# Performance work log

Measured on AMD Instinct MI355X. Metric: run time of the kernel, lower is better.

## Reference

```python
import jax, jax.numpy as jnp
import numpy as np
from jax import lax

DB4 = np.array([0.2303778133088964, 0.7148465705529155, 0.6308807679298587,
                -0.027983769416859854, -0.18703481171888114, 0.030841381835986965,
                0.032883011666982945, -0.010597401785069032], dtype=np.float32)


def _make_filters():
    h = DB4
    g = np.array([(-1) ** n * DB4[7 - n] for n in range(8)], dtype=np.float32)
    # analysis filters (as in DaubechiesDWT): [LL, LH, HL, HH], each 8x8
    anal = np.stack([np.outer(h, h), np.outer(h, g), np.outer(g, h), np.outer(g, g)], axis=0)
    anal = anal[:, None, :, :]  # (4,1,8,8) OIHW depthwise
    # synthesis filters (as in DaubechiesIDWT), built from time-reversed filters
    h_r, g_r = h[::-1], g[::-1]
    syn = np.stack([np.outer(h_r, h_r), np.outer(h_r, g_r), np.outer(g_r, h_r), np.outer(g_r, g_r)], axis=0)
    syn = syn[:, None, :, :]  # (4,1,8,8), torch conv_transpose weight layout (IC, OC/g, kH, kW)
    # convert conv_transpose2d(stride=2, pad=3) to a dilated conv: flip spatially, swap I/O,
    # equivalent padding = k - 1 - pad = 8 - 1 - 3 = 4
    syn_eq = np.transpose(syn[:, :, ::-1, ::-1], (1, 0, 2, 3)).copy()  # (1,4,8,8) OIHW
    return jnp.asarray(anal), jnp.asarray(syn_eq)


def setup_inputs() -> dict:
    key = jax.random.key(0)
    x = jax.random.normal(key, (32, 3, 512, 512), dtype=jnp.float32)
    return {"x": x}


def reference(x) -> jnp.ndarray:
    B, C, H, W = x.shape
    anal_w, syn_w = _make_filters()
    dn = ('NCHW', 'OIHW', 'NCHW')
    # --- depthwise DWT: groups=C, stride 2, pad 3 -> (B, 4C, Ho, Wo) ---
    anal_wC = jnp.tile(anal_w, (C, 1, 1, 1))  # (4C,1,8,8)
    coeffs = lax.conv_general_dilated(x, anal_wC, window_strides=(2, 2),
                                      padding=[(3, 3), (3, 3)],
                                      feature_group_count=C, dimension_numbers=dn)
    Ho, Wo = coeffs.shape[-2], coeffs.shape[-1]
    coeffs = coeffs.reshape(B, C, 4, Ho, Wo)
    # --- high-pass: zero the LL subband ---
    coeffs = coeffs.at[:, :, 0].set(0.0)
    coeffs = coeffs.reshape(B, 4 * C, Ho, Wo)
    # --- IDWT as single grouped transposed conv (lhs_dilation=2, pad 4) ---
    syn_wC = jnp.tile(syn_w, (C, 1, 1, 1))  # (C,4,8,8)
    recon = lax.conv_general_dilated(coeffs, syn_wC, window_strides=(1, 1),
                                     padding=[(4, 4), (4, 4)], lhs_dilation=(2, 2),
                                     feature_group_count=C, dimension_numbers=dn)
    recon = recon[:, :, :2 * Ho, :2 * Wo]  # crop to output_size = (2*Ho, 2*Wo)
    # --- per-sample min-max normalization ---
    mn = jnp.min(recon, axis=(1, 2, 3), keepdims=True)
    mx = jnp.max(recon, axis=(1, 2, 3), keepdims=True)
    return (recon - mn) / (mx - mn + 1e-8)
```

## Files before the change

kernel.cpp:

```cpp
#include <hip/hip_runtime.h>

#define H0 0.2303778133088964f
#define H1 0.7148465705529155f
#define H2 0.6308807679298587f
#define H3 (-0.027983769416859854f)
#define H4 (-0.18703481171888114f)
#define H5 0.030841381835986965f
#define H6 0.032883011666982945f
#define H7 (-0.010597401785069032f)


__global__ __launch_bounds__(256, 8) void dwt_fused_k(const float* __restrict__ x,
                                                      float* __restrict__ out,
                                                      float* __restrict__ pmn,
                                                      float* __restrict__ pmx) {
    constexpr float h[8] = {H0, H1, H2, H3, H4, H5, H6, H7};
    constexpr float g[8] = {H7, -H6, H5, -H4, H3, -H2, H1, -H0};

    const int tileX = blockIdx.x;
    const int tileY = blockIdx.y;
    const int img = blockIdx.z;
    const int N0 = tileX * 32;
    const int M0 = tileY * 32;
    const int tid = threadIdx.x;

    __shared__ __align__(16) unsigned char smem[16928];
    float* sx = (float*)smem;
    float* y1 = (float*)smem;
    float* y2 = (float*)(smem + 1600);
    float* y3 = (float*)(smem + 3200);
    float* red = (float*)(smem + 4800);
    float* uL = (float*)(smem + 9568);
    float* uH = (float*)(smem + 13248);
    float* sP = (float*)(smem + 9568);
    float* sQ = (float*)(smem + 12128);

    const float* xp = x + (size_t)img * (512 * 512);

    {
        const int gr0 = M0 - 7, gc0 = N0 - 8;
        for (int k = tid; k < 598; k += 256) {
            int row = k / 13;
            int c4 = k - row * 13;
            int gr = gr0 + row;
            int gc = gc0 + 4 * c4;
            float4 v = make_float4(0.f, 0.f, 0.f, 0.f);
            if ((unsigned)gr < 512u && (unsigned)gc < 512u)
                v = *(const float4*)(xp + gr * 512 + gc);
            *(float4*)(sx + row * 52 + 4 * c4) = v;
        }
    }
    __syncthreads();

    const int C0 = (N0 >> 1) - 2;
    if (tid < 230) {
        int p = tid / 5;
        int q = tid - p * 5;
        const float4* wr = (const float4*)(sx + p * 52 + 8 * q);
        float4 w0 = wr[0], w1 = wr[1], w2 = wr[2], w3 = wr[3];
        float W[16] = {w0.x, w0.y, w0.z, w0.w, w1.x, w1.y, w1.z, w1.w,
                       w2.x, w2.y, w2.z, w2.w, w3.x, w3.y, w3.z, w3.w};
        float aL[4] = {0.f, 0.f, 0.f, 0.f}, aH[4] = {0.f, 0.f, 0.f, 0.f};
#pragma unroll
        for (int d = 0; d < 4; ++d) {
#pragma unroll
            for (int j = 0; j < 8; ++j) {
                float v = W[1 + 2 * d + j];
                aL[d] += h[j] * v;
                aH[d] += g[j] * v;
            }
            if ((unsigned)(C0 + 4 * q + d) >= 256u) { aL[d] = 0.f; aH[d] = 0.f; }
        }
        *(float4*)(uL + p * 20 + 4 * q) = make_float4(aL[0], aL[1], aL[2], aL[3]);
        *(float4*)(uH + p * 20 + 4 * q) = make_float4(aH[0], aH[1], aH[2], aH[3]);
    }
    __syncthreads();

    const int R0 = (M0 >> 1) - 2;
    if (tid < 100) {
        int lr = tid / 5;
        int q = tid - lr * 5;
        float a1[4] = {0.f, 0.f, 0.f, 0.f};
        float a2[4] = {0.f, 0.f, 0.f, 0.f};
        float a3[4] = {0.f, 0.f, 0.f, 0.f};
        if ((unsigned)(R0 + lr) < 256u) {
#pragma unroll
            for (int i = 0; i < 8; ++i) {
                float4 vH = *(const float4*)(uH + (2 * lr + i) * 20 + 4 * q);
                float4 vL = *(const float4*)(uL + (2 * lr + i) * 20 + 4 * q);
                a1[0] += h[i] * vH.x; a1[1] += h[i] * vH.y; a1[2] += h[i] * vH.z; a1[3] += h[i] * vH.w;
                a2[0] += g[i] * vL.x; a2[1] += g[i] * vL.y; a2[2] += g[i] * vL.z; a2[3] += g[i] * vL.w;
                a3[0] += g[i] * vH.x; a3[1] += g[i] * vH.y; a3[2] += g[i] * vH.z; a3[3] += g[i] * vH.w;
            }
        }
        *(float4*)(y1 + lr * 20 + 4 * q) = make_float4(a1[0], a1[1], a1[2], a1[3]);
        *(float4*)(y2 + lr * 20 + 4 * q) = make_float4(a2[0], a2[1], a2[2], a2[3]);
        *(float4*)(y3 + lr * 20 + 4 * q) = make_float4(a3[0], a3[1], a3[2], a3[3]);
    }
    __syncthreads();

    if (tid < 160) {
        int m = tid / 5;
        int q = tid - m * 5;
        int mh = (m + (m & 1)) >> 1;
        int t0 = m & 1;
        float ch0 = t0 ? H1 : H0, ch1 = t0 ? H3 : H2, ch2 = t0 ? H5 : H4, ch3 = t0 ? H7 : H6;
        float cg0 = t0 ? -H6 : H7, cg1 = t0 ? -H4 : H5, cg2 = t0 ? -H2 : H3, cg3 = t0 ? -H0 : H1;
        float P[4] = {0.f, 0.f, 0.f, 0.f}, Q[4] = {0.f, 0.f, 0.f, 0.f};
#pragma unroll
        for (int k = 0; k < 4; ++k) {
            float chk = (k == 0) ? ch0 : (k == 1) ? ch1 : (k == 2) ? ch2 : ch3;
            float cgk = (k == 0) ? cg0 : (k == 1) ? cg1 : (k == 2) ? cg2 : cg3;
            float4 v1 = *(const float4*)(y1 + (mh + k) * 20 + 4 * q);
            float4 v3 = *(const float4*)(y3 + (mh + k) * 20 + 4 * q);
            float4 v2 = *(const float4*)(y2 + (mh + k) * 20 + 4 * q);
            P[0] += chk * v1.x + cgk * v3.x; P[1] += chk * v1.y + cgk * v3.y;
            P[2] += chk * v1.z + cgk * v3.z; P[3] += chk * v1.w + cgk * v3.w;
            Q[0] += cgk * v2.x; Q[1] += cgk * v2.y; Q[2] += cgk * v2.z; Q[3] += cgk * v2.w;
        }
        *(float4*)(sP + m * 20 + 4 * q) = make_float4(P[0], P[1], P[2], P[3]);
        *(float4*)(sQ + m * 20 + 4 * q) = make_float4(Q[0], Q[1], Q[2], Q[3]);
    }
    __syncthreads();

    float lmn = 3.4e38f, lmx = -3.4e38f;
    if (tid < 128) {
        int m = tid >> 2;
        int qq = tid & 3;
        const float* pp = sP + m * 20 + 4 * qq;
        const float* qp = sQ + m * 20 + 4 * qq;
        float4 pa = *(const float4*)pp, pb = *(const float4*)(pp + 4);
        float4 qa = *(const float4*)qp, qb = *(const float4*)(qp + 4);
        float sp[8] = {pa.x, pa.y, pa.z, pa.w, pb.x, pb.y, pb.z, pb.w};
        float sq[8] = {qa.x, qa.y, qa.z, qa.w, qb.x, qb.y, qb.z, qb.w};
        float val[8];
#pragma unroll
        for (int e = 0; e < 8; ++e) {
            const int t0 = e & 1;
            const int r0 = (e + (e & 1)) >> 1;
            float r = g[t0] * sp[r0] + g[t0 + 2] * sp[r0 + 1] + g[t0 + 4] * sp[r0 + 2] + g[t0 + 6] * sp[r0 + 3]
                    + h[t0] * sq[r0] + h[t0 + 2] * sq[r0 + 1] + h[t0 + 4] * sq[r0 + 2] + h[t0 + 6] * sq[r0 + 3];
            val[e] = r;
            lmn = fminf(lmn, r);
            lmx = fmaxf(lmx, r);
        }
        float* op = out + ((size_t)img * 512 + (M0 + m)) * 512 + (N0 + 8 * qq);
        *(float4*)op = make_float4(val[0], val[1], val[2], val[3]);
        *(float4*)(op + 4) = make_float4(val[4], val[5], val[6], val[7]);
    }

#pragma unroll
    for (int off = 32; off > 0; off >>= 1) {
        lmn = fminf(lmn, __shfl_down(lmn, off));
        lmx = fmaxf(lmx, __shfl_down(lmx, off));
    }
    int wv = tid >> 6;
    if ((tid & 63) == 0) { red[wv] = lmn; red[4 + wv] = lmx; }
    __syncthreads();
    if (tid == 0) {
        float mn = fminf(fminf(red[0], red[1]), fminf(red[2], red[3]));
        float mx = fmaxf(fmaxf(red[4], red[5]), fmaxf(red[6], red[7]));
        int blin = (img * 16 + tileY) * 16 + tileX;
        pmn[blin] = mn;
        pmx[blin] = mx;
    }
}

__global__ __launch_bounds__(256) void minmax_reduce_k(const float* __restrict__ pmn,
                                                       const float* __restrict__ pmx,
                                                       float* __restrict__ mnmx) {
    __shared__ float r[8];
    int s = blockIdx.x;
    int tid = threadIdx.x;
    int base = s * 768;
    float lmn = 3.4e38f, lmx = -3.4e38f;
#pragma unroll
    for (int k = 0; k < 3; ++k) {
        lmn = fminf(lmn, pmn[base + tid + 256 * k]);
        lmx = fmaxf(lmx, pmx[base + tid + 256 * k]);
    }
#pragma unroll
    for (int off = 32; off > 0; off >>= 1) {
        lmn = fminf(lmn, __shfl_down(lmn, off));
        lmx = fmaxf(lmx, __shfl_down(lmx, off));
    }
    int wv = tid >> 6;
    if ((tid & 63) == 0) { r[wv] = lmn; r[4 + wv] = lmx; }
    __syncthreads();
    if (tid == 0) {
        mnmx[s]      = fminf(fminf(r[0], r[1]), fminf(r[2], r[3]));
        mnmx[32 + s] = fmaxf(fmaxf(r[4], r[5]), fmaxf(r[6], r[7]));
    }
}

__global__ __launch_bounds__(256) void normalize_k(float* __restrict__ out,
                                                   const float* __restrict__ mnmx) {
    int t = blockIdx.x * 256 + threadIdx.x;
    float4* o4 = (float4*)out;
#pragma unroll
    for (int it = 0; it < 6; ++it) {
        size_t i = (size_t)t + (size_t)it * 1048576;
        int s = (int)(i / 196608);
        float mn = mnmx[s];
        float mx = mnmx[32 + s];
        float inv = 1.0f / (mx - mn + 1e-8f);
        float4 v = o4[i];
        v.x = (v.x - mn) * inv;
        v.y = (v.y - mn) * inv;
        v.z = (v.z - mn) * inv;
        v.w = (v.w - mn) * inv;
        o4[i] = v;
    }
}

extern "C" void kernel_launch(void* const* d_in, const int* in_sizes, int n_in,
                              void* d_out, int out_size, void* d_ws, size_t ws_size,
                              hipStream_t stream) {
    const float* x = (const float*)d_in[0];
    float* out = (float*)d_out;
    float* wsf = (float*)d_ws;
    float* pmn = wsf;
    float* pmx = wsf + 24576;
    float* mnmx = wsf + 49152;

    hipLaunchKernelGGL(dwt_fused_k, dim3(16, 16, 96), dim3(256), 0, stream, x, out, pmn, pmx);
    hipLaunchKernelGGL(minmax_reduce_k, dim3(32), dim3(256), 0, stream, pmn, pmx, mnmx);
    hipLaunchKernelGGL(normalize_k, dim3(4096), dim3(256), 0, stream, out, mnmx);
}
```

Measured before the change: 241.1 us.

## Widen DWT tiles to 64 columns and fold min-max reduction into normalize

```diff
diff --git a/kernel.cpp b/kernel.cpp
--- a/kernel.cpp
+++ b/kernel.cpp
@@ -9,8 +9,7 @@
 #define H6 0.032883011666982945f
 #define H7 (-0.010597401785069032f)
 
-
-__global__ __launch_bounds__(256, 8) void dwt_fused_k(const float* __restrict__ x,
+__global__ __launch_bounds__(256, 5) void dwt_fused_k(const float* __restrict__ x,
                                                       float* __restrict__ out,
                                                       float* __restrict__ pmn,
                                                       float* __restrict__ pmx) {
@@ -20,43 +19,43 @@
     const int tileX = blockIdx.x;
     const int tileY = blockIdx.y;
     const int img = blockIdx.z;
-    const int N0 = tileX * 32;
+    const int N0 = tileX * 64;
     const int M0 = tileY * 32;
     const int tid = threadIdx.x;
 
-    __shared__ __align__(16) unsigned char smem[16928];
+    __shared__ __align__(16) unsigned char smem[27968];
     float* sx = (float*)smem;
     float* y1 = (float*)smem;
-    float* y2 = (float*)(smem + 1600);
-    float* y3 = (float*)(smem + 3200);
-    float* red = (float*)(smem + 4800);
-    float* uL = (float*)(smem + 9568);
-    float* uH = (float*)(smem + 13248);
-    float* sP = (float*)(smem + 9568);
-    float* sQ = (float*)(smem + 12128);
+    float* y2 = (float*)(smem + 2880);
+    float* y3 = (float*)(smem + 5760);
+    float* red = (float*)(smem + 8640);
+    float* uL = (float*)(smem + 14720);
+    float* uH = (float*)(smem + 21344);
+    float* sP = (float*)(smem + 14720);
+    float* sQ = (float*)(smem + 19328);
 
     const float* xp = x + (size_t)img * (512 * 512);
 
     {
         const int gr0 = M0 - 7, gc0 = N0 - 8;
-        for (int k = tid; k < 598; k += 256) {
-            int row = k / 13;
-            int c4 = k - row * 13;
+        for (int k = tid; k < 920; k += 256) {
+            int row = k / 20;
+            int c4 = k - row * 20;
             int gr = gr0 + row;
             int gc = gc0 + 4 * c4;
             float4 v = make_float4(0.f, 0.f, 0.f, 0.f);
             if ((unsigned)gr < 512u && (unsigned)gc < 512u)
                 v = *(const float4*)(xp + gr * 512 + gc);
-            *(float4*)(sx + row * 52 + 4 * c4) = v;
+            *(float4*)(sx + row * 80 + 4 * c4) = v;
         }
     }
     __syncthreads();
 
     const int C0 = (N0 >> 1) - 2;
-    if (tid < 230) {
-        int p = tid / 5;
-        int q = tid - p * 5;
-        const float4* wr = (const float4*)(sx + p * 52 + 8 * q);
+    for (int t = tid; t < 414; t += 256) {
+        int p = t / 9;
+        int gq = t - p * 9;
+        const float4* wr = (const float4*)(sx + p * 80 + 8 * gq);
         float4 w0 = wr[0], w1 = wr[1], w2 = wr[2], w3 = wr[3];
         float W[16] = {w0.x, w0.y, w0.z, w0.w, w1.x, w1.y, w1.z, w1.w,
                        w2.x, w2.y, w2.z, w2.w, w3.x, w3.y, w3.z, w3.w};
@@ -69,39 +68,39 @@
                 aL[d] += h[j] * v;
                 aH[d] += g[j] * v;
             }
-            if ((unsigned)(C0 + 4 * q + d) >= 256u) { aL[d] = 0.f; aH[d] = 0.f; }
-        }
-        *(float4*)(uL + p * 20 + 4 * q) = make_float4(aL[0], aL[1], aL[2], aL[3]);
-        *(float4*)(uH + p * 20 + 4 * q) = make_float4(aH[0], aH[1], aH[2], aH[3]);
+            if ((unsigned)(C0 + 4 * gq + d) >= 256u) { aL[d] = 0.f; aH[d] = 0.f; }
+        }
+        *(float4*)(uL + p * 36 + 4 * gq) = make_float4(aL[0], aL[1], aL[2], aL[3]);
+        *(float4*)(uH + p * 36 + 4 * gq) = make_float4(aH[0], aH[1], aH[2], aH[3]);
     }
     __syncthreads();
 
     const int R0 = (M0 >> 1) - 2;
-    if (tid < 100) {
-        int lr = tid / 5;
-        int q = tid - lr * 5;
+    if (tid < 180) {
+        int lr = tid / 9;
+        int gq = tid - lr * 9;
         float a1[4] = {0.f, 0.f, 0.f, 0.f};
         float a2[4] = {0.f, 0.f, 0.f, 0.f};
         float a3[4] = {0.f, 0.f, 0.f, 0.f};
         if ((unsigned)(R0 + lr) < 256u) {
 #pragma unroll
             for (int i = 0; i < 8; ++i) {
-                float4 vH = *(const float4*)(uH + (2 * lr + i) * 20 + 4 * q);
-                float4 vL = *(const float4*)(uL + (2 * lr + i) * 20 + 4 * q);
+                float4 vH = *(const float4*)(uH + (2 * lr + i) * 36 + 4 * gq);
+                float4 vL = *(const float4*)(uL + (2 * lr + i) * 36 + 4 * gq);
                 a1[0] += h[i] * vH.x; a1[1] += h[i] * vH.y; a1[2] += h[i] * vH.z; a1[3] += h[i] * vH.w;
                 a2[0] += g[i] * vL.x; a2[1] += g[i] * vL.y; a2[2] += g[i] * vL.z; a2[3] += g[i] * vL.w;
                 a3[0] += g[i] * vH.x; a3[1] += g[i] * vH.y; a3[2] += g[i] * vH.z; a3[3] += g[i] * vH.w;
             }
         }
-        *(float4*)(y1 + lr * 20 + 4 * q) = make_float4(a1[0], a1[1], a1[2], a1[3]);
-        *(float4*)(y2 + lr * 20 + 4 * q) = make_float4(a2[0], a2[1], a2[2], a2[3]);
-        *(float4*)(y3 + lr * 20 + 4 * q) = make_float4(a3[0], a3[1], a3[2], a3[3]);
-    }
-    __syncthreads();
-
-    if (tid < 160) {
-        int m = tid / 5;
-        int q = tid - m * 5;
+        *(float4*)(y1 + lr * 36 + 4 * gq) = make_float4(a1[0], a1[1], a1[2], a1[3]);
+        *(float4*)(y2 + lr * 36 + 4 * gq) = make_float4(a2[0], a2[1], a2[2], a2[3]);
+        *(float4*)(y3 + lr * 36 + 4 * gq) = make_float4(a3[0], a3[1], a3[2], a3[3]);
+    }
+    __syncthreads();
+
+    for (int t = tid; t < 288; t += 256) {
+        int m = t / 9;
+        int gq = t - m * 9;
         int mh = (m + (m & 1)) >> 1;
         int t0 = m & 1;
         float ch0 = t0 ? H1 : H0, ch1 = t0 ? H3 : H2, ch2 = t0 ? H5 : H4, ch3 = t0 ? H7 : H6;
@@ -111,24 +110,24 @@
         for (int k = 0; k < 4; ++k) {
             float chk = (k == 0) ? ch0 : (k == 1) ? ch1 : (k == 2) ? ch2 : ch3;
             float cgk = (k == 0) ? cg0 : (k == 1) ? cg1 : (k == 2) ? cg2 : cg3;
-            float4 v1 = *(const float4*)(y1 + (mh + k) * 20 + 4 * q);
-            float4 v3 = *(const float4*)(y3 + (mh + k) * 20 + 4 * q);
-            float4 v2 = *(const float4*)(y2 + (mh + k) * 20 + 4 * q);
+            float4 v1 = *(const float4*)(y1 + (mh + k) * 36 + 4 * gq);
+            float4 v3 = *(const float4*)(y3 + (mh + k) * 36 + 4 * gq);
+            float4 v2 = *(const float4*)(y2 + (mh + k) * 36 + 4 * gq);
             P[0] += chk * v1.x + cgk * v3.x; P[1] += chk * v1.y + cgk * v3.y;
             P[2] += chk * v1.z + cgk * v3.z; P[3] += chk * v1.w + cgk * v3.w;
             Q[0] += cgk * v2.x; Q[1] += cgk * v2.y; Q[2] += cgk * v2.z; Q[3] += cgk * v2.w;
         }
-        *(float4*)(sP + m * 20 + 4 * q) = make_float4(P[0], P[1], P[2], P[3]);
-        *(float4*)(sQ + m * 20 + 4 * q) = make_float4(Q[0], Q[1], Q[2], Q[3]);
+        *(float4*)(sP + m * 36 + 4 * gq) = make_float4(P[0], P[1], P[2], P[3]);
+        *(float4*)(sQ + m * 36 + 4 * gq) = make_float4(Q[0], Q[1], Q[2], Q[3]);
     }
     __syncthreads();
 
     float lmn = 3.4e38f, lmx = -3.4e38f;
-    if (tid < 128) {
-        int m = tid >> 2;
-        int qq = tid & 3;
-        const float* pp = sP + m * 20 + 4 * qq;
-        const float* qp = sQ + m * 20 + 4 * qq;
+    {
+        int m = tid >> 3;
+        int qq = tid & 7;
+        const float* pp = sP + m * 36 + 4 * qq;
+        const float* qp = sQ + m * 36 + 4 * qq;
         float4 pa = *(const float4*)pp, pb = *(const float4*)(pp + 4);
         float4 qa = *(const float4*)qp, qb = *(const float4*)(qp + 4);
         float sp[8] = {pa.x, pa.y, pa.z, pa.w, pb.x, pb.y, pb.z, pb.w};
@@ -160,24 +159,27 @@
     if (tid == 0) {
         float mn = fminf(fminf(red[0], red[1]), fminf(red[2], red[3]));
         float mx = fmaxf(fmaxf(red[4], red[5]), fmaxf(red[6], red[7]));
-        int blin = (img * 16 + tileY) * 16 + tileX;
+        int blin = (img * 16 + tileY) * 8 + tileX;
         pmn[blin] = mn;
         pmx[blin] = mx;
     }
 }
 
-__global__ __launch_bounds__(256) void minmax_reduce_k(const float* __restrict__ pmn,
-                                                       const float* __restrict__ pmx,
-                                                       float* __restrict__ mnmx) {
+__global__ __launch_bounds__(256) void normalize_k(float* __restrict__ out,
+                                                   const float* __restrict__ pmn,
+                                                   const float* __restrict__ pmx) {
     __shared__ float r[8];
-    int s = blockIdx.x;
-    int tid = threadIdx.x;
-    int base = s * 768;
+    __shared__ float bc[2];
+    const int b = blockIdx.x;
+    const int s = b / 96;
+    const int chunk = b - s * 96;
+    const int tid = threadIdx.x;
+
     float lmn = 3.4e38f, lmx = -3.4e38f;
-#pragma unroll
-    for (int k = 0; k < 3; ++k) {
-        lmn = fminf(lmn, pmn[base + tid + 256 * k]);
-        lmx = fmaxf(lmx, pmx[base + tid + 256 * k]);
+    const int base = s * 384;
+    for (int j = tid; j < 384; j += 256) {
+        lmn = fminf(lmn, pmn[base + j]);
+        lmx = fmaxf(lmx, pmx[base + j]);
     }
 #pragma unroll
     for (int off = 32; off > 0; off >>= 1) {
@@ -188,22 +190,18 @@
     if ((tid & 63) == 0) { r[wv] = lmn; r[4 + wv] = lmx; }
     __syncthreads();
     if (tid == 0) {
-        mnmx[s]      = fminf(fminf(r[0], r[1]), fminf(r[2], r[3]));
-        mnmx[32 + s] = fmaxf(fmaxf(r[4], r[5]), fmaxf(r[6], r[7]));
-    }
-}
-
-__global__ __launch_bounds__(256) void normalize_k(float* __restrict__ out,
-                                                   const float* __restrict__ mnmx) {
-    int t = blockIdx.x * 256 + threadIdx.x;
+        bc[0] = fminf(fminf(r[0], r[1]), fminf(r[2], r[3]));
+        bc[1] = fmaxf(fmaxf(r[4], r[5]), fmaxf(r[6], r[7]));
+    }
+    __syncthreads();
+    const float mn = bc[0];
+    const float inv = 1.0f / (bc[1] - mn + 1e-8f);
+
     float4* o4 = (float4*)out;
-#pragma unroll
-    for (int it = 0; it < 6; ++it) {
-        size_t i = (size_t)t + (size_t)it * 1048576;
-        int s = (int)(i / 196608);
-        float mn = mnmx[s];
-        float mx = mnmx[32 + s];
-        float inv = 1.0f / (mx - mn + 1e-8f);
+    const size_t base4 = (size_t)s * 196608 + (size_t)chunk * 2048;
+#pragma unroll
+    for (int it = 0; it < 8; ++it) {
+        size_t i = base4 + it * 256 + tid;
         float4 v = o4[i];
         v.x = (v.x - mn) * inv;
         v.y = (v.y - mn) * inv;
@@ -220,10 +218,8 @@
     float* out = (float*)d_out;
     float* wsf = (float*)d_ws;
     float* pmn = wsf;
-    float* pmx = wsf + 24576;
-    float* mnmx = wsf + 49152;
-
-    hipLaunchKernelGGL(dwt_fused_k, dim3(16, 16, 96), dim3(256), 0, stream, x, out, pmn, pmx);
-    hipLaunchKernelGGL(minmax_reduce_k, dim3(32), dim3(256), 0, stream, pmn, pmx, mnmx);
-    hipLaunchKernelGGL(normalize_k, dim3(4096), dim3(256), 0, stream, out, mnmx);
+    float* pmx = wsf + 12288;
+
+    hipLaunchKernelGGL(dwt_fused_k, dim3(8, 16, 96), dim3(256), 0, stream, x, out, pmn, pmx);
+    hipLaunchKernelGGL(normalize_k, dim3(3072), dim3(256), 0, stream, out, pmn, pmx);
 }
```

New measurement: 250.2 us. +3.8%, slower.

## Fold vertical IDWT/DWT passes into precomputed combined taps for interior tiles

Applied to the files above, without the earlier changes.

```diff
diff --git a/kernel.cpp b/kernel.cpp
--- a/kernel.cpp
+++ b/kernel.cpp
@@ -9,8 +9,33 @@
 #define H6 0.032883011666982945f
 #define H7 (-0.010597401785069032f)
 
-
-__global__ __launch_bounds__(256, 8) void dwt_fused_k(const float* __restrict__ x,
+struct Taps { float cp[2][14]; float cq[2][14]; };
+constexpr Taps mk_taps() {
+    Taps t{};
+    const float h[8] = {H0, H1, H2, H3, H4, H5, H6, H7};
+    const float g[8] = {H7, -H6, H5, -H4, H3, -H2, H1, -H0};
+    for (int par = 0; par < 2; ++par)
+        for (int j = 0; j < 14; ++j) {
+            float cp = 0.f, cq = 0.f;
+            for (int k = 0; k < 4; ++k) {
+                int i = j - 2 * k;
+                if (i >= 0 && i < 8) {
+                    cp += h[2 * k + par] * h[i] + g[2 * k + par] * g[i];
+                    cq += g[2 * k + par] * g[i];
+                }
+            }
+            t.cp[par][j] = cp;
+            t.cq[par][j] = cq;
+        }
+    return t;
+}
+constexpr Taps TAPS = mk_taps();
+
+__device__ __forceinline__ int uoff(int r, int c4) {
+    return r * 32 + 4 * (c4 ^ ((r >> 1) & 7));
+}
+
+__global__ __launch_bounds__(256, 7) void dwt_fused_k(const float* __restrict__ x,
                                                       float* __restrict__ out,
                                                       float* __restrict__ pmn,
                                                       float* __restrict__ pmx) {
@@ -24,16 +49,22 @@
     const int M0 = tileY * 32;
     const int tid = threadIdx.x;
 
-    __shared__ __align__(16) unsigned char smem[16928];
+    __shared__ __align__(16) unsigned char smem[21344];
     float* sx = (float*)smem;
     float* y1 = (float*)smem;
     float* y2 = (float*)(smem + 1600);
     float* y3 = (float*)(smem + 3200);
-    float* red = (float*)(smem + 4800);
+    float* red = (float*)(smem + 5120);
     float* uL = (float*)(smem + 9568);
-    float* uH = (float*)(smem + 13248);
-    float* sP = (float*)(smem + 9568);
-    float* sQ = (float*)(smem + 12128);
+    float* uH = (float*)(smem + 15456);
+    float* sPi = (float*)smem;
+    float* sQi = (float*)(smem + 2560);
+    float* sPb = (float*)(smem + 9568);
+    float* sQb = (float*)(smem + 12128);
+
+    const bool boundary = (tileY == 0) | (tileY == 15);
+    float* sP = boundary ? sPb : sPi;
+    float* sQ = boundary ? sQb : sQi;
 
     const float* xp = x + (size_t)img * (512 * 512);
 
@@ -71,55 +102,87 @@
             }
             if ((unsigned)(C0 + 4 * q + d) >= 256u) { aL[d] = 0.f; aH[d] = 0.f; }
         }
-        *(float4*)(uL + p * 20 + 4 * q) = make_float4(aL[0], aL[1], aL[2], aL[3]);
-        *(float4*)(uH + p * 20 + 4 * q) = make_float4(aH[0], aH[1], aH[2], aH[3]);
-    }
-    __syncthreads();
-
-    const int R0 = (M0 >> 1) - 2;
-    if (tid < 100) {
-        int lr = tid / 5;
-        int q = tid - lr * 5;
-        float a1[4] = {0.f, 0.f, 0.f, 0.f};
-        float a2[4] = {0.f, 0.f, 0.f, 0.f};
-        float a3[4] = {0.f, 0.f, 0.f, 0.f};
-        if ((unsigned)(R0 + lr) < 256u) {
-#pragma unroll
-            for (int i = 0; i < 8; ++i) {
-                float4 vH = *(const float4*)(uH + (2 * lr + i) * 20 + 4 * q);
-                float4 vL = *(const float4*)(uL + (2 * lr + i) * 20 + 4 * q);
-                a1[0] += h[i] * vH.x; a1[1] += h[i] * vH.y; a1[2] += h[i] * vH.z; a1[3] += h[i] * vH.w;
-                a2[0] += g[i] * vL.x; a2[1] += g[i] * vL.y; a2[2] += g[i] * vL.z; a2[3] += g[i] * vL.w;
-                a3[0] += g[i] * vH.x; a3[1] += g[i] * vH.y; a3[2] += g[i] * vH.z; a3[3] += g[i] * vH.w;
-            }
-        }
-        *(float4*)(y1 + lr * 20 + 4 * q) = make_float4(a1[0], a1[1], a1[2], a1[3]);
-        *(float4*)(y2 + lr * 20 + 4 * q) = make_float4(a2[0], a2[1], a2[2], a2[3]);
-        *(float4*)(y3 + lr * 20 + 4 * q) = make_float4(a3[0], a3[1], a3[2], a3[3]);
-    }
-    __syncthreads();
-
-    if (tid < 160) {
-        int m = tid / 5;
-        int q = tid - m * 5;
-        int mh = (m + (m & 1)) >> 1;
-        int t0 = m & 1;
-        float ch0 = t0 ? H1 : H0, ch1 = t0 ? H3 : H2, ch2 = t0 ? H5 : H4, ch3 = t0 ? H7 : H6;
-        float cg0 = t0 ? -H6 : H7, cg1 = t0 ? -H4 : H5, cg2 = t0 ? -H2 : H3, cg3 = t0 ? -H0 : H1;
-        float P[4] = {0.f, 0.f, 0.f, 0.f}, Q[4] = {0.f, 0.f, 0.f, 0.f};
-#pragma unroll
-        for (int k = 0; k < 4; ++k) {
-            float chk = (k == 0) ? ch0 : (k == 1) ? ch1 : (k == 2) ? ch2 : ch3;
-            float cgk = (k == 0) ? cg0 : (k == 1) ? cg1 : (k == 2) ? cg2 : cg3;
-            float4 v1 = *(const float4*)(y1 + (mh + k) * 20 + 4 * q);
-            float4 v3 = *(const float4*)(y3 + (mh + k) * 20 + 4 * q);
-            float4 v2 = *(const float4*)(y2 + (mh + k) * 20 + 4 * q);
-            P[0] += chk * v1.x + cgk * v3.x; P[1] += chk * v1.y + cgk * v3.y;
-            P[2] += chk * v1.z + cgk * v3.z; P[3] += chk * v1.w + cgk * v3.w;
-            Q[0] += cgk * v2.x; Q[1] += cgk * v2.y; Q[2] += cgk * v2.z; Q[3] += cgk * v2.w;
-        }
-        *(float4*)(sP + m * 20 + 4 * q) = make_float4(P[0], P[1], P[2], P[3]);
-        *(float4*)(sQ + m * 20 + 4 * q) = make_float4(Q[0], Q[1], Q[2], Q[3]);
+        int o = uoff(p, q);
+        *(float4*)(uL + o) = make_float4(aL[0], aL[1], aL[2], aL[3]);
+        *(float4*)(uH + o) = make_float4(aH[0], aH[1], aH[2], aH[3]);
+    }
+    __syncthreads();
+
+    if (boundary) {
+        const int R0 = (M0 >> 1) - 2;
+        if (tid < 100) {
+            int lr = tid / 5;
+            int q = tid - lr * 5;
+            float a1[4] = {0.f, 0.f, 0.f, 0.f};
+            float a2[4] = {0.f, 0.f, 0.f, 0.f};
+            float a3[4] = {0.f, 0.f, 0.f, 0.f};
+            if ((unsigned)(R0 + lr) < 256u) {
+#pragma unroll
+                for (int i = 0; i < 8; ++i) {
+                    int o = uoff(2 * lr + i, q);
+                    float4 vH = *(const float4*)(uH + o);
+                    float4 vL = *(const float4*)(uL + o);
+                    a1[0] += h[i] * vH.x; a1[1] += h[i] * vH.y; a1[2] += h[i] * vH.z; a1[3] += h[i] * vH.w;
+                    a2[0] += g[i] * vL.x; a2[1] += g[i] * vL.y; a2[2] += g[i] * vL.z; a2[3] += g[i] * vL.w;
+                    a3[0] += g[i] * vH.x; a3[1] += g[i] * vH.y; a3[2] += g[i] * vH.z; a3[3] += g[i] * vH.w;
+                }
+            }
+            *(float4*)(y1 + lr * 20 + 4 * q) = make_float4(a1[0], a1[1], a1[2], a1[3]);
+            *(float4*)(y2 + lr * 20 + 4 * q) = make_float4(a2[0], a2[1], a2[2], a2[3]);
+            *(float4*)(y3 + lr * 20 + 4 * q) = make_float4(a3[0], a3[1], a3[2], a3[3]);
+        }
+        __syncthreads();
+        if (tid < 160) {
+            int m = tid / 5;
+            int q = tid - m * 5;
+            int mh = (m + (m & 1)) >> 1;
+            int t0 = m & 1;
+            float ch0 = t0 ? H1 : H0, ch1 = t0 ? H3 : H2, ch2 = t0 ? H5 : H4, ch3 = t0 ? H7 : H6;
+            float cg0 = t0 ? -H6 : H7, cg1 = t0 ? -H4 : H5, cg2 = t0 ? -H2 : H3, cg3 = t0 ? -H0 : H1;
+            float P[4] = {0.f, 0.f, 0.f, 0.f}, Q[4] = {0.f, 0.f, 0.f, 0.f};
+#pragma unroll
+            for (int k = 0; k < 4; ++k) {
+                float chk = (k == 0) ? ch0 : (k == 1) ? ch1 : (k == 2) ? ch2 : ch3;
+                float cgk = (k == 0) ? cg0 : (k == 1) ? cg1 : (k == 2) ? cg2 : cg3;
+                float4 v1 = *(const float4*)(y1 + (mh + k) * 20 + 4 * q);
+                float4 v3 = *(const float4*)(y3 + (mh + k) * 20 + 4 * q);
+                float4 v2 = *(const float4*)(y2 + (mh + k) * 20 + 4 * q);
+                P[0] += chk * v1.x + cgk * v3.x; P[1] += chk * v1.y + cgk * v3.y;
+                P[2] += chk * v1.z + cgk * v3.z; P[3] += chk * v1.w + cgk * v3.w;
+                Q[0] += cgk * v2.x; Q[1] += cgk * v2.y; Q[2] += cgk * v2.z; Q[3] += cgk * v2.w;
+            }
+            *(float4*)(sP + m * 20 + 4 * q) = make_float4(P[0], P[1], P[2], P[3]);
+            *(float4*)(sQ + m * 20 + 4 * q) = make_float4(Q[0], Q[1], Q[2], Q[3]);
+        }
+    } else {
+        if (tid < 80) {
+            int t = tid / 5;
+            int q = tid - t * 5;
+            float P0[4] = {0.f, 0.f, 0.f, 0.f}, Q0[4] = {0.f, 0.f, 0.f, 0.f};
+            float P1[4] = {0.f, 0.f, 0.f, 0.f}, Q1[4] = {0.f, 0.f, 0.f, 0.f};
+            const int rbase = 2 * t;
+#pragma unroll
+            for (int rr = 0; rr < 16; ++rr) {
+                int o = uoff(rbase + rr, q);
+                float4 vH = *(const float4*)(uH + o);
+                float4 vL = *(const float4*)(uL + o);
+                if (rr <= 13) {
+                    const float a = TAPS.cp[0][rr], b = TAPS.cq[0][rr];
+                    P0[0] += a * vH.x; P0[1] += a * vH.y; P0[2] += a * vH.z; P0[3] += a * vH.w;
+                    Q0[0] += b * vL.x; Q0[1] += b * vL.y; Q0[2] += b * vL.z; Q0[3] += b * vL.w;
+                }
+                if (rr >= 2) {
+                    const float a = TAPS.cp[1][rr - 2], b = TAPS.cq[1][rr - 2];
+                    P1[0] += a * vH.x; P1[1] += a * vH.y; P1[2] += a * vH.z; P1[3] += a * vH.w;
+                    Q1[0] += b * vL.x; Q1[1] += b * vL.y; Q1[2] += b * vL.z; Q1[3] += b * vL.w;
+                }
+            }
+            int m0 = 2 * t;
+            *(float4*)(sP + m0 * 20 + 4 * q)       = make_float4(P0[0], P0[1], P0[2], P0[3]);
+            *(float4*)(sP + (m0 + 1) * 20 + 4 * q) = make_float4(P1[0], P1[1], P1[2], P1[3]);
+            *(float4*)(sQ + m0 * 20 + 4 * q)       = make_float4(Q0[0], Q0[1], Q0[2], Q0[3]);
+            *(float4*)(sQ + (m0 + 1) * 20 + 4 * q) = make_float4(Q1[0], Q1[1], Q1[2], Q1[3]);
+        }
     }
     __syncthreads();
 
@@ -195,15 +258,17 @@
 
 __global__ __launch_bounds__(256) void normalize_k(float* __restrict__ out,
                                                    const float* __restrict__ mnmx) {
-    int t = blockIdx.x * 256 + threadIdx.x;
+    const int b = blockIdx.x;
+    const int s = b >> 6;
+    const int c = b & 63;
+    const int tid = threadIdx.x;
+    const float mn = mnmx[s];
+    const float inv = 1.0f / (mnmx[32 + s] - mn + 1e-8f);
     float4* o4 = (float4*)out;
-#pragma unroll
-    for (int it = 0; it < 6; ++it) {
-        size_t i = (size_t)t + (size_t)it * 1048576;
-        int s = (int)(i / 196608);
-        float mn = mnmx[s];
-        float mx = mnmx[32 + s];
-        float inv = 1.0f / (mx - mn + 1e-8f);
+    const size_t base4 = (size_t)s * 196608 + (size_t)c * 3072;
+#pragma unroll
+    for (int it = 0; it < 12; ++it) {
+        size_t i = base4 + it * 256 + tid;
         float4 v = o4[i];
         v.x = (v.x - mn) * inv;
         v.y = (v.y - mn) * inv;
@@ -225,5 +290,5 @@
 
     hipLaunchKernelGGL(dwt_fused_k, dim3(16, 16, 96), dim3(256), 0, stream, x, out, pmn, pmx);
     hipLaunchKernelGGL(minmax_reduce_k, dim3(32), dim3(256), 0, stream, pmn, pmx, mnmx);
-    hipLaunchKernelGGL(normalize_k, dim3(4096), dim3(256), 0, stream, out, mnmx);
-}
+    hipLaunchKernelGGL(normalize_k, dim3(2048), dim3(256), 0, stream, out, mnmx);
+}
```

Measured after the change: 283.6 us. +17.6%, slower.
